# Kernel optimization log

Measured on AMD Instinct MI355X. Metric: run time of the kernel, lower is better.

Reference implementation:

```python
import jax, jax.numpy as jnp
import numpy as np

N = 100000
E = 1600000
C_IN = 128
C_OUT = 128
EPS = 1e-5


def setup_inputs() -> dict:
    key = jax.random.key(0)
    ks = jax.random.split(key, 8)
    x = jax.random.normal(ks[0], (N, C_IN), dtype=jnp.float32)
    edge_index = jax.random.randint(ks[1], (2, E), 0, N, dtype=jnp.int64)
    s_proj = 1.0 / np.sqrt(C_IN)
    s_out = 1.0 / np.sqrt(C_IN)
    W_proj = jax.random.uniform(ks[2], (C_IN, C_IN), jnp.float32, -s_proj, s_proj)
    b_proj = jax.random.uniform(ks[3], (C_IN,), jnp.float32, -s_proj, s_proj)
    W_l = jax.random.uniform(ks[4], (C_OUT, C_IN), jnp.float32, -s_out, s_out)
    b_l = jax.random.uniform(ks[5], (C_OUT,), jnp.float32, -s_out, s_out)
    W_r = jax.random.uniform(ks[6], (C_OUT, C_IN), jnp.float32, -s_out, s_out)
    gamma = jnp.ones((C_OUT,), jnp.float32)
    beta = jnp.zeros((C_OUT,), jnp.float32)
    return {"x": x, "edge_index": edge_index, "W_proj": W_proj, "b_proj": b_proj,
            "W_l": W_l, "b_l": b_l, "W_r": W_r, "gamma": gamma, "beta": beta}


def reference(x, edge_index, W_proj, b_proj, W_l, b_l, W_r, gamma, beta):
    # SAGEConv(project=True, aggr='sum'): project+ReLU source features per node,
    # gather along edges, scatter-sum at targets, then lin_l(agg) + lin_r(x_root).
    src, dst = edge_index[0], edge_index[1]
    h = jax.nn.relu(x @ W_proj.T + b_proj)            # [N, C_IN]
    msg = h[src]                                       # [E, C_IN] edge gather
    agg = jax.ops.segment_sum(msg, dst, num_segments=N)  # [N, C_IN]
    out = agg @ W_l.T + b_l + x @ W_r.T                # [N, C_OUT] (root uses unprojected x)
    # LayerNorm(c_out)
    mu = jnp.mean(out, axis=-1, keepdims=True)
    var = jnp.var(out, axis=-1, keepdims=True)
    return (out - mu) * jax.lax.rsqrt(var + EPS) * gamma + beta
```

## Files before the change

### kernel.cpp

```cpp
#include <hip/hip_runtime.h>
#include <stdint.h>

#define NN 100000
#define NE 1600000
#define C  128
#define NB 782
#define CAP 4096
#define SB_SHIFT 13
#define MB 782
#define P1B 250
#define MBO 782

typedef __attribute__((ext_vector_type(8))) short short8;
typedef __attribute__((ext_vector_type(4))) float f32x4;

__device__ __forceinline__ float bf2f(uint16_t u) {
  union { uint32_t u; float f; } v; v.u = ((uint32_t)u) << 16; return v.f;
}
__device__ __forceinline__ uint16_t f2bf(float f) {
  union { float f; uint32_t u; } v; v.f = f;
  uint32_t r = v.u + 0x7fffu + ((v.u >> 16) & 1u);
  return (uint16_t)(r >> 16);
}
__device__ __forceinline__ float2 bf2x2(uint32_t u) {
  return make_float2(bf2f((uint16_t)u), bf2f((uint16_t)(u >> 16)));
}

__global__ __launch_bounds__(256) void cast3_k(
    const float* __restrict__ a, const float* __restrict__ b, const float* __restrict__ c,
    uint16_t* __restrict__ oa, uint16_t* __restrict__ ob, uint16_t* __restrict__ oc)
{
  int i = blockIdx.x * 256 + threadIdx.x;
  int which = i >> 12, j = i & 4095;
  const float* s = which == 0 ? a : (which == 1 ? b : c);
  uint16_t* d    = which == 0 ? oa : (which == 1 ? ob : oc);
  float4 v = ((const float4*)s)[j];
  uint2 p;
  p.x = (uint32_t)f2bf(v.x) | ((uint32_t)f2bf(v.y) << 16);
  p.y = (uint32_t)f2bf(v.z) | ((uint32_t)f2bf(v.w) << 16);
  ((uint2*)d)[j] = p;
}


__global__ __launch_bounds__(512) void fused_front_k(
    const float* __restrict__ x, const uint16_t* __restrict__ wpb,
    const uint16_t* __restrict__ wrb,
    const float* __restrict__ bp, const float* __restrict__ bl,
    uint16_t* __restrict__ h, uint16_t* __restrict__ rb,
    const int* __restrict__ esrc, const int* __restrict__ edst,
    int* __restrict__ gcnt, uint32_t* __restrict__ ebuf)
{
  extern __shared__ uint8_t slds[];
  const int t = threadIdx.x;

  if (blockIdx.x < MB) {
#pragma unroll
    for (int qq = 0; qq < 8; ++qq) {
      int ci = qq * 512 + t;
      int m  = ci >> 11;
      int cj = ci & 2047;
      int cl = cj >> 4, k16 = cj & 15;
      const uint16_t* wsrc = m == 0 ? wpb : wrb;
      *(short8*)(slds + m * 32768 + cl * 256 + ((k16 ^ (cl & 15)) << 4)) =
          *(const short8*)(wsrc + cj * 8);
    }
    __syncthreads();

    const int w = t >> 6, lane = t & 63;
    const int tile_m0 = blockIdx.x * 128;
    const int r16 = lane & 15, g = lane >> 4;
    const int row = tile_m0 + w * 16 + r16;
    const int arow = row < NN ? row : NN - 1;

    short8 a[4];
    const float* xp = x + (size_t)arow * C + g * 8;
#pragma unroll
    for (int kk = 0; kk < 4; ++kk) {
      float4 u = *(const float4*)(xp + kk * 32);
      float4 v = *(const float4*)(xp + kk * 32 + 4);
      short8 av;
      av[0] = (short)f2bf(u.x); av[1] = (short)f2bf(u.y);
      av[2] = (short)f2bf(u.z); av[3] = (short)f2bf(u.w);
      av[4] = (short)f2bf(v.x); av[5] = (short)f2bf(v.y);
      av[6] = (short)f2bf(v.z); av[7] = (short)f2bf(v.w);
      a[kk] = av;
    }

    f32x4 hp[8], hr[8];
#pragma unroll
    for (int nt = 0; nt < 8; ++nt) {
      f32x4 p = {0.f, 0.f, 0.f, 0.f};
      f32x4 r = {0.f, 0.f, 0.f, 0.f};
      const int cidx = nt * 16 + r16;
      const uint8_t* rbp = slds + cidx * 256;
      const uint8_t* rbr = slds + 32768 + cidx * 256;
#pragma unroll
      for (int kk = 0; kk < 4; ++kk) {
        int slot = (((kk << 2) + g) ^ (cidx & 15)) << 4;
        p = __builtin_amdgcn_mfma_f32_16x16x32_bf16(*(const short8*)(rbp + slot), a[kk], p, 0, 0, 0);
        r = __builtin_amdgcn_mfma_f32_16x16x32_bf16(*(const short8*)(rbr + slot), a[kk], r, 0, 0, 0);
      }
      hp[nt] = p; hr[nt] = r;
    }
    __syncthreads();

    const int lrow = w * 16 + r16;
#pragma unroll
    for (int nt = 0; nt < 8; ++nt) {
      const int col0 = nt * 16 + g * 4;
      float4 bp4 = *(const float4*)(bp + col0);
      float4 bl4 = *(const float4*)(bl + col0);
      float h0 = hp[nt][0] + bp4.x, h1 = hp[nt][1] + bp4.y;
      float h2 = hp[nt][2] + bp4.z, h3 = hp[nt][3] + bp4.w;
      h0 = h0 > 0.f ? h0 : 0.f; h1 = h1 > 0.f ? h1 : 0.f;
      h2 = h2 > 0.f ? h2 : 0.f; h3 = h3 > 0.f ? h3 : 0.f;
      uint2 ph, pr;
      ph.x = (uint32_t)f2bf(h0) | ((uint32_t)f2bf(h1) << 16);
      ph.y = (uint32_t)f2bf(h2) | ((uint32_t)f2bf(h3) << 16);
      pr.x = (uint32_t)f2bf(hr[nt][0] + bl4.x) | ((uint32_t)f2bf(hr[nt][1] + bl4.y) << 16);
      pr.y = (uint32_t)f2bf(hr[nt][2] + bl4.z) | ((uint32_t)f2bf(hr[nt][3] + bl4.w) << 16);
      const int ioff = (col0 * 2) ^ ((lrow & 15) << 4);
      *(uint2*)(slds + lrow * 256 + ioff) = ph;
      *(uint2*)(slds + 32768 + lrow * 256 + ioff) = pr;
    }
    __syncthreads();

#pragma unroll
    for (int i = 0; i < 4; ++i) {
      const int ofs = i * 8192 + t * 16;
      const int trow = ofs >> 8;
      const int inrow = ofs & 255;
      const int grow = tile_m0 + trow;
      const int phys = (trow << 8) + (inrow ^ ((trow & 15) << 4));
      if (grow < NN) {
        *(uint4*)(h  + (size_t)grow * C + (inrow >> 1)) = *(const uint4*)(slds + phys);
        *(uint4*)(rb + (size_t)grow * C + (inrow >> 1)) = *(const uint4*)(slds + 32768 + phys);
      }
    }
  } else {
    int* bh = (int*)slds;
    int* gb = bh + NB;
    const int blk = blockIdx.x - MB;
    const int base = blk * 6400;

    for (int i = t; i < NB; i += 512) bh[i] = 0;

    const int4* ed4 = (const int4*)(edst + base);
    const int4* es4 = (const int4*)(esrc + base);
    int4 dv[4], sv[4];
    bool val[4];
#pragma unroll
    for (int k = 0; k < 4; ++k) {
      int i = t + k * 512;
      val[k] = (i < 1600);
      if (val[k]) { dv[k] = ed4[i]; sv[k] = es4[i]; }
    }
    __syncthreads();

#pragma unroll
    for (int k = 0; k < 4; ++k) if (val[k]) {
      atomicAdd(&bh[dv[k].x >> 7], 1); atomicAdd(&bh[dv[k].y >> 7], 1);
      atomicAdd(&bh[dv[k].z >> 7], 1); atomicAdd(&bh[dv[k].w >> 7], 1);
    }
    __syncthreads();

    for (int i = t; i < NB; i += 512) {
      int c = bh[i];
      gb[i] = c ? atomicAdd(&gcnt[i], c) : 0;
      bh[i] = 0;
    }
    __syncthreads();

#define P1_SCATTER(d, s) do { \
      int bb = (d) >> 7; \
      int o = atomicAdd(&bh[bb], 1); \
      int pos = gb[bb] + o; \
      if (pos < CAP) ebuf[(size_t)bb * CAP + pos] = ((uint32_t)((d) & 127) << 17) | (uint32_t)(s); \
    } while (0)

#pragma unroll
    for (int k = 0; k < 4; ++k) if (val[k]) {
      P1_SCATTER(dv[k].x, sv[k].x); P1_SCATTER(dv[k].y, sv[k].y);
      P1_SCATTER(dv[k].z, sv[k].z); P1_SCATTER(dv[k].w, sv[k].w);
    }
#undef P1_SCATTER
  }
}

__global__ __launch_bounds__(256) void phase2_k(
    const uint32_t* __restrict__ ebuf, const int* __restrict__ gcnt,
    int* __restrict__ ssrc, int2* __restrict__ sdeg)
{
  __shared__ uint32_t raw[CAP];
  __shared__ int lout[CAP];
  __shared__ int cnt2[128 * 16];
  __shared__ int nd[128];
  __shared__ int psum[256];
  const int b = blockIdx.x, t = threadIdx.x;
  const int n0 = b * 128;

  int acc = 0;
  for (int i = t; i < b; i += 256) acc += gcnt[i];
  psum[t] = acc;
  __syncthreads();
  for (int off = 128; off > 0; off >>= 1) {
    if (t < off) psum[t] += psum[t + off];
    __syncthreads();
  }
  const int base = psum[0];
  int cnt = gcnt[b]; if (cnt > CAP) cnt = CAP;

  for (int i = t; i < 128 * 16; i += 256) cnt2[i] = 0;
  __syncthreads();
  for (int i = t; i < cnt; i += 256) {
    uint32_t v = ebuf[(size_t)b * CAP + i];
    raw[i] = v;
    atomicAdd(&cnt2[(v >> 17) * 16 + ((v & 0x1FFFFu) >> SB_SHIFT)], 1);
  }
  __syncthreads();

  int deg_t = 0;
  if (t < 128) {
#pragma unroll
    for (int i = 0; i < 16; ++i) deg_t += cnt2[t * 16 + i];
    nd[t] = deg_t;
  }
  __syncthreads();
  for (int off = 1; off < 128; off <<= 1) {
    int v = 0;
    if (t < 128 && t >= off) v = nd[t - off];
    __syncthreads();
    if (t < 128) nd[t] += v;
    __syncthreads();
  }
  if (t < 128) {
    int pref = nd[t] - deg_t;
    if (n0 + t < NN) sdeg[n0 + t] = make_int2(base + pref, deg_t);
    int run = pref;
#pragma unroll
    for (int i = 0; i < 16; ++i) { int c = cnt2[t * 16 + i]; cnt2[t * 16 + i] = run; run += c; }
  }
  __syncthreads();
  for (int i = t; i < cnt; i += 256) {
    uint32_t v = raw[i];
    int o = atomicAdd(&cnt2[(v >> 17) * 16 + ((v & 0x1FFFFu) >> SB_SHIFT)], 1);
    lout[o] = (int)(v & 0x1FFFFu);
  }
  __syncthreads();
  for (int i = t; i < cnt; i += 256) ssrc[base + i] = lout[i];
}

__global__ __launch_bounds__(256) void aggregate_k(
    const uint16_t* __restrict__ h, const int* __restrict__ ssrc,
    const int2* __restrict__ sdeg, uint16_t* __restrict__ agg)
{
  const int wid = (blockIdx.x * 256 + threadIdx.x) >> 6;
  if (wid >= NN) return;
  const int lane = threadIdx.x & 63;
  const int q = lane >> 4;
  const int l16 = lane & 15;
  const int2 sd = sdeg[wid];
  const int s0 = sd.x, cnt = sd.y;
  const size_t choff = (size_t)l16 * 8;
  float2 a0 = {0.f, 0.f}, a1 = {0.f, 0.f}, a2 = {0.f, 0.f}, a3 = {0.f, 0.f};

#define ACC8(v) do { \
    a0 += bf2x2((v).x); a1 += bf2x2((v).y); \
    a2 += bf2x2((v).z); a3 += bf2x2((v).w); \
  } while (0)

  if (cnt > 0) {
    int e0 = ssrc[s0 + ((q      < cnt) ? q      : cnt - 1)];
    int e1 = ssrc[s0 + ((q + 4  < cnt) ? q + 4  : cnt - 1)];
    int e2 = ssrc[s0 + ((q + 8  < cnt) ? q + 8  : cnt - 1)];
    int e3 = ssrc[s0 + ((q + 12 < cnt) ? q + 12 : cnt - 1)];
    for (int j = 0; j < cnt; j += 16) {
      uint4 v0 = *(const uint4*)(h + (size_t)e0 * C + choff);
      uint4 v1 = *(const uint4*)(h + (size_t)e1 * C + choff);
      uint4 v2 = *(const uint4*)(h + (size_t)e2 * C + choff);
      uint4 v3 = *(const uint4*)(h + (size_t)e3 * C + choff);
      const int jn = j + 16;
      if (jn < cnt) {
        e0 = ssrc[s0 + ((jn + q      < cnt) ? jn + q      : cnt - 1)];
        e1 = ssrc[s0 + ((jn + q + 4  < cnt) ? jn + q + 4  : cnt - 1)];
        e2 = ssrc[s0 + ((jn + q + 8  < cnt) ? jn + q + 8  : cnt - 1)];
        e3 = ssrc[s0 + ((jn + q + 12 < cnt) ? jn + q + 12 : cnt - 1)];
      }
      if (j + q      < cnt) ACC8(v0);
      if (j + q + 4  < cnt) ACC8(v1);
      if (j + q + 8  < cnt) ACC8(v2);
      if (j + q + 12 < cnt) ACC8(v3);
    }
  }
#undef ACC8

#pragma unroll
  for (int msk = 16; msk <= 32; msk <<= 1) {
    a0.x += __shfl_xor(a0.x, msk, 64); a0.y += __shfl_xor(a0.y, msk, 64);
    a1.x += __shfl_xor(a1.x, msk, 64); a1.y += __shfl_xor(a1.y, msk, 64);
    a2.x += __shfl_xor(a2.x, msk, 64); a2.y += __shfl_xor(a2.y, msk, 64);
    a3.x += __shfl_xor(a3.x, msk, 64); a3.y += __shfl_xor(a3.y, msk, 64);
  }
  if (q == 0) {
    uint4 p;
    p.x = (uint32_t)f2bf(a0.x) | ((uint32_t)f2bf(a0.y) << 16);
    p.y = (uint32_t)f2bf(a1.x) | ((uint32_t)f2bf(a1.y) << 16);
    p.z = (uint32_t)f2bf(a2.x) | ((uint32_t)f2bf(a2.y) << 16);
    p.w = (uint32_t)f2bf(a3.x) | ((uint32_t)f2bf(a3.y) << 16);
    *(uint4*)(agg + (size_t)wid * C + choff) = p;
  }
}

__global__ __launch_bounds__(512) void gemm_out_k(
    const uint16_t* __restrict__ aggb, const uint16_t* __restrict__ rb,
    const uint16_t* __restrict__ wlb, const float* __restrict__ gamma,
    const float* __restrict__ beta, float* __restrict__ out)
{
  __shared__ uint8_t wl[32768];
  const int t = threadIdx.x;
#pragma unroll
  for (int qq = 0; qq < 4; ++qq) {
    int ci = qq * 512 + t;
    int c = ci >> 4, k16 = ci & 15;
    *(short8*)(wl + c * 256 + ((k16 ^ (c & 15)) << 4)) = *(const short8*)(wlb + ci * 8);
  }
  __syncthreads();

  const int w = t >> 6, lane = t & 63;
  const int tile_m = blockIdx.x * 128 + w * 16;
  if (tile_m >= NN) return;
  const int r16 = lane & 15, g = lane >> 4;

  const int row = tile_m + r16;
  const int arow = row < NN ? row : NN - 1;
  short8 a0[4];
  const uint16_t* p0 = aggb + (size_t)arow * C + g * 8;
#pragma unroll
  for (int kk = 0; kk < 4; ++kk) a0[kk] = *(const short8*)(p0 + kk * 32);

  f32x4 acc[8];
  float s1 = 0.f, s2 = 0.f;
#pragma unroll
  for (int nt = 0; nt < 8; ++nt) {
    f32x4 c4 = {0.f, 0.f, 0.f, 0.f};
    const int c = nt * 16 + r16;
    const uint8_t* rbl = wl + c * 256;
#pragma unroll
    for (int kk = 0; kk < 4; ++kk) {
      short8 b = *(const short8*)(rbl + ((((kk << 2) + g) ^ (c & 15)) << 4));
      c4 = __builtin_amdgcn_mfma_f32_16x16x32_bf16(b, a0[kk], c4, 0, 0, 0);
    }
    const int col0 = nt * 16 + g * 4;
    uint2 rv = *(const uint2*)(rb + (size_t)arow * C + col0);
    float2 r01 = bf2x2(rv.x), r23 = bf2x2(rv.y);
    c4[0] += r01.x; c4[1] += r01.y; c4[2] += r23.x; c4[3] += r23.y;
#pragma unroll
    for (int rr = 0; rr < 4; ++rr) { s1 += c4[rr]; s2 += c4[rr] * c4[rr]; }
    acc[nt] = c4;
  }

  s1 += __shfl_xor(s1, 16, 64); s2 += __shfl_xor(s2, 16, 64);
  s1 += __shfl_xor(s1, 32, 64); s2 += __shfl_xor(s2, 32, 64);
  const float mean = s1 * (1.f / C);
  const float var = s2 * (1.f / C) - mean * mean;
  const float rstd = rsqrtf(var + 1e-5f);

  if (row < NN) {
#pragma unroll
    for (int nt = 0; nt < 8; ++nt) {
      const int col0 = nt * 16 + g * 4;
      float4 gm = *(const float4*)(gamma + col0);
      float4 bt = *(const float4*)(beta + col0);
      float4 o;
      o.x = (acc[nt][0] - mean) * rstd * gm.x + bt.x;
      o.y = (acc[nt][1] - mean) * rstd * gm.y + bt.y;
      o.z = (acc[nt][2] - mean) * rstd * gm.z + bt.z;
      o.w = (acc[nt][3] - mean) * rstd * gm.w + bt.w;
      *(float4*)(out + (size_t)row * C + col0) = o;
    }
  }
}

extern "C" void kernel_launch(void* const* d_in, const int* in_sizes, int n_in,
                              void* d_out, int out_size, void* d_ws, size_t ws_size,
                              hipStream_t stream)
{
  const float* x        = (const float*)d_in[0];
  const int* ei         = (const int*)d_in[1];
  const float* Wp       = (const float*)d_in[2];
  const float* bp       = (const float*)d_in[3];
  const float* Wl       = (const float*)d_in[4];
  const float* bl       = (const float*)d_in[5];
  const float* Wr       = (const float*)d_in[6];
  const float* gamma    = (const float*)d_in[7];
  const float* beta     = (const float*)d_in[8];
  float* out            = (float*)d_out;

  char* ws = (char*)d_ws;
  uint16_t* rb   = (uint16_t*)(ws + 0);
  uint16_t* h    = (uint16_t*)(ws + 25600000);
  uint32_t* ebuf = (uint32_t*)(ws + 51200000);
  uint16_t* aggb = (uint16_t*)(ws + 51200000);
  uint16_t* wpb  = (uint16_t*)(ws + 76800000);
  uint16_t* wlb  = (uint16_t*)(ws + 76832768);
  uint16_t* wrb  = (uint16_t*)(ws + 76865536);
  int2* sdeg     = (int2*)(ws + 76898304);
  int* gcnt      = (int*)(ws + 77698304);
  int* ssrc      = (int*)(ws + 78102400);

  const int* esrc = ei;
  const int* edst = ei + NE;

  hipMemsetAsync(gcnt, 0, NB * sizeof(int), stream);

  cast3_k<<<48, 256, 0, stream>>>(Wp, Wl, Wr, wpb, wlb, wrb);

  fused_front_k<<<MB + P1B, 512, 65536, stream>>>(
      x, wpb, wrb, bp, bl, h, rb, esrc, edst, gcnt, ebuf);

  phase2_k<<<NB, 256, 0, stream>>>(ebuf, gcnt, ssrc, sdeg);

  aggregate_k<<<(NN + 3) / 4, 256, 0, stream>>>(h, ssrc, sdeg, aggb);

  gemm_out_k<<<MBO, 512, 0, stream>>>(aggb, rb, wlb, gamma, beta, out);
}
```

Before: 141.0 us.

## Move root GEMM x@W_r into output GEMM, drop rb buffer; split aggregate tail

The root projection x@W_r.T, previously computed in the front kernel and stored as a bf16 intermediate, is now computed in the output GEMM. That kernel rereads x in fp32, converts it to bf16 and accumulates both GEMMs into the same MFMA accumulators. This removes writing and rereading a 25.6MB intermediate, and cuts front-kernel LDS from 64KB to 32KB. The output kernel now needs 64KB of LDS and reads 51MB of fp32 x. The aggregate kernel also gets an unpredicated main loop over full 16-edge chunks plus a separate remainder step, removing per-iteration clamping and predication.

```diff
diff --git a/kernel.cpp b/kernel.cpp
--- a/kernel.cpp
+++ b/kernel.cpp
@@ -25,6 +25,16 @@
 __device__ __forceinline__ float2 bf2x2(uint32_t u) {
   return make_float2(bf2f((uint16_t)u), bf2f((uint16_t)(u >> 16)));
 }
+__device__ __forceinline__ short8 cvt_row8(const float* p) {
+  float4 u = *(const float4*)p;
+  float4 v = *(const float4*)(p + 4);
+  short8 av;
+  av[0] = (short)f2bf(u.x); av[1] = (short)f2bf(u.y);
+  av[2] = (short)f2bf(u.z); av[3] = (short)f2bf(u.w);
+  av[4] = (short)f2bf(v.x); av[5] = (short)f2bf(v.y);
+  av[6] = (short)f2bf(v.z); av[7] = (short)f2bf(v.w);
+  return av;
+}
 
 __global__ __launch_bounds__(256) void cast3_k(
     const float* __restrict__ a, const float* __restrict__ b, const float* __restrict__ c,
@@ -44,9 +54,7 @@
 
 __global__ __launch_bounds__(512) void fused_front_k(
     const float* __restrict__ x, const uint16_t* __restrict__ wpb,
-    const uint16_t* __restrict__ wrb,
-    const float* __restrict__ bp, const float* __restrict__ bl,
-    uint16_t* __restrict__ h, uint16_t* __restrict__ rb,
+    const float* __restrict__ bp, uint16_t* __restrict__ h,
     const int* __restrict__ esrc, const int* __restrict__ edst,
     int* __restrict__ gcnt, uint32_t* __restrict__ ebuf)
 {
@@ -55,14 +63,11 @@
 
   if (blockIdx.x < MB) {
 #pragma unroll
-    for (int qq = 0; qq < 8; ++qq) {
+    for (int qq = 0; qq < 4; ++qq) {
       int ci = qq * 512 + t;
-      int m  = ci >> 11;
-      int cj = ci & 2047;
-      int cl = cj >> 4, k16 = cj & 15;
-      const uint16_t* wsrc = m == 0 ? wpb : wrb;
-      *(short8*)(slds + m * 32768 + cl * 256 + ((k16 ^ (cl & 15)) << 4)) =
-          *(const short8*)(wsrc + cj * 8);
+      int cl = ci >> 4, k16 = ci & 15;
+      *(short8*)(slds + cl * 256 + ((k16 ^ (cl & 15)) << 4)) =
+          *(const short8*)(wpb + ci * 8);
     }
     __syncthreads();
 
@@ -75,32 +80,20 @@
     short8 a[4];
     const float* xp = x + (size_t)arow * C + g * 8;
 #pragma unroll
-    for (int kk = 0; kk < 4; ++kk) {
-      float4 u = *(const float4*)(xp + kk * 32);
-      float4 v = *(const float4*)(xp + kk * 32 + 4);
-      short8 av;
-      av[0] = (short)f2bf(u.x); av[1] = (short)f2bf(u.y);
-      av[2] = (short)f2bf(u.z); av[3] = (short)f2bf(u.w);
-      av[4] = (short)f2bf(v.x); av[5] = (short)f2bf(v.y);
-      av[6] = (short)f2bf(v.z); av[7] = (short)f2bf(v.w);
-      a[kk] = av;
-    }
-
-    f32x4 hp[8], hr[8];
+    for (int kk = 0; kk < 4; ++kk) a[kk] = cvt_row8(xp + kk * 32);
+
+    f32x4 hp[8];
 #pragma unroll
     for (int nt = 0; nt < 8; ++nt) {
       f32x4 p = {0.f, 0.f, 0.f, 0.f};
-      f32x4 r = {0.f, 0.f, 0.f, 0.f};
       const int cidx = nt * 16 + r16;
       const uint8_t* rbp = slds + cidx * 256;
-      const uint8_t* rbr = slds + 32768 + cidx * 256;
 #pragma unroll
       for (int kk = 0; kk < 4; ++kk) {
         int slot = (((kk << 2) + g) ^ (cidx & 15)) << 4;
         p = __builtin_amdgcn_mfma_f32_16x16x32_bf16(*(const short8*)(rbp + slot), a[kk], p, 0, 0, 0);
-        r = __builtin_amdgcn_mfma_f32_16x16x32_bf16(*(const short8*)(rbr + slot), a[kk], r, 0, 0, 0);
       }
-      hp[nt] = p; hr[nt] = r;
+      hp[nt] = p;
     }
     __syncthreads();
 
@@ -109,19 +102,14 @@
     for (int nt = 0; nt < 8; ++nt) {
       const int col0 = nt * 16 + g * 4;
       float4 bp4 = *(const float4*)(bp + col0);
-      float4 bl4 = *(const float4*)(bl + col0);
       float h0 = hp[nt][0] + bp4.x, h1 = hp[nt][1] + bp4.y;
       float h2 = hp[nt][2] + bp4.z, h3 = hp[nt][3] + bp4.w;
       h0 = h0 > 0.f ? h0 : 0.f; h1 = h1 > 0.f ? h1 : 0.f;
       h2 = h2 > 0.f ? h2 : 0.f; h3 = h3 > 0.f ? h3 : 0.f;
-      uint2 ph, pr;
+      uint2 ph;
       ph.x = (uint32_t)f2bf(h0) | ((uint32_t)f2bf(h1) << 16);
       ph.y = (uint32_t)f2bf(h2) | ((uint32_t)f2bf(h3) << 16);
-      pr.x = (uint32_t)f2bf(hr[nt][0] + bl4.x) | ((uint32_t)f2bf(hr[nt][1] + bl4.y) << 16);
-      pr.y = (uint32_t)f2bf(hr[nt][2] + bl4.z) | ((uint32_t)f2bf(hr[nt][3] + bl4.w) << 16);
-      const int ioff = (col0 * 2) ^ ((lrow & 15) << 4);
-      *(uint2*)(slds + lrow * 256 + ioff) = ph;
-      *(uint2*)(slds + 32768 + lrow * 256 + ioff) = pr;
+      *(uint2*)(slds + lrow * 256 + ((col0 * 2) ^ ((lrow & 15) << 4))) = ph;
     }
     __syncthreads();
 
@@ -131,11 +119,9 @@
       const int trow = ofs >> 8;
       const int inrow = ofs & 255;
       const int grow = tile_m0 + trow;
-      const int phys = (trow << 8) + (inrow ^ ((trow & 15) << 4));
-      if (grow < NN) {
-        *(uint4*)(h  + (size_t)grow * C + (inrow >> 1)) = *(const uint4*)(slds + phys);
-        *(uint4*)(rb + (size_t)grow * C + (inrow >> 1)) = *(const uint4*)(slds + 32768 + phys);
-      }
+      if (grow < NN)
+        *(uint4*)(h + (size_t)grow * C + (inrow >> 1)) =
+            *(const uint4*)(slds + (trow << 8) + (inrow ^ ((trow & 15) << 4)));
     }
   } else {
     int* bh = (int*)slds;
@@ -269,28 +255,45 @@
     a2 += bf2x2((v).z); a3 += bf2x2((v).w); \
   } while (0)
 
-  if (cnt > 0) {
-    int e0 = ssrc[s0 + ((q      < cnt) ? q      : cnt - 1)];
-    int e1 = ssrc[s0 + ((q + 4  < cnt) ? q + 4  : cnt - 1)];
-    int e2 = ssrc[s0 + ((q + 8  < cnt) ? q + 8  : cnt - 1)];
-    int e3 = ssrc[s0 + ((q + 12 < cnt) ? q + 12 : cnt - 1)];
-    for (int j = 0; j < cnt; j += 16) {
+  int j = 0;
+  if (cnt >= 16) {
+    int e0 = ssrc[s0 + q];
+    int e1 = ssrc[s0 + 4 + q];
+    int e2 = ssrc[s0 + 8 + q];
+    int e3 = ssrc[s0 + 12 + q];
+    for (; j + 16 <= cnt;) {
       uint4 v0 = *(const uint4*)(h + (size_t)e0 * C + choff);
       uint4 v1 = *(const uint4*)(h + (size_t)e1 * C + choff);
       uint4 v2 = *(const uint4*)(h + (size_t)e2 * C + choff);
       uint4 v3 = *(const uint4*)(h + (size_t)e3 * C + choff);
-      const int jn = j + 16;
-      if (jn < cnt) {
-        e0 = ssrc[s0 + ((jn + q      < cnt) ? jn + q      : cnt - 1)];
-        e1 = ssrc[s0 + ((jn + q + 4  < cnt) ? jn + q + 4  : cnt - 1)];
-        e2 = ssrc[s0 + ((jn + q + 8  < cnt) ? jn + q + 8  : cnt - 1)];
-        e3 = ssrc[s0 + ((jn + q + 12 < cnt) ? jn + q + 12 : cnt - 1)];
+      j += 16;
+      if (j + 16 <= cnt) {
+        e0 = ssrc[s0 + j + q];
+        e1 = ssrc[s0 + j + 4 + q];
+        e2 = ssrc[s0 + j + 8 + q];
+        e3 = ssrc[s0 + j + 12 + q];
       }
-      if (j + q      < cnt) ACC8(v0);
-      if (j + q + 4  < cnt) ACC8(v1);
-      if (j + q + 8  < cnt) ACC8(v2);
-      if (j + q + 12 < cnt) ACC8(v3);
-    }
+      ACC8(v0); ACC8(v1); ACC8(v2); ACC8(v3);
+    }
+  }
+  const int rem = cnt - j;
+  if (rem > 0) {
+    int i0 = j + ((q      < rem) ? q      : 0);
+    int i1 = j + ((q + 4  < rem) ? q + 4  : 0);
+    int i2 = j + ((q + 8  < rem) ? q + 8  : 0);
+    int i3 = j + ((q + 12 < rem) ? q + 12 : 0);
+    int e0 = ssrc[s0 + i0];
+    int e1 = ssrc[s0 + i1];
+    int e2 = ssrc[s0 + i2];
+    int e3 = ssrc[s0 + i3];
+    uint4 v0 = *(const uint4*)(h + (size_t)e0 * C + choff);
+    uint4 v1 = *(const uint4*)(h + (size_t)e1 * C + choff);
+    uint4 v2 = *(const uint4*)(h + (size_t)e2 * C + choff);
+    uint4 v3 = *(const uint4*)(h + (size_t)e3 * C + choff);
+    if (q < rem)      ACC8(v0);
+    if (q + 4 < rem)  ACC8(v1);
+    if (q + 8 < rem)  ACC8(v2);
+    if (q + 12 < rem) ACC8(v3);
   }
 #undef ACC8
 
@@ -312,17 +315,22 @@
 }
 
 __global__ __launch_bounds__(512) void gemm_out_k(
-    const uint16_t* __restrict__ aggb, const uint16_t* __restrict__ rb,
-    const uint16_t* __restrict__ wlb, const float* __restrict__ gamma,
+    const uint16_t* __restrict__ aggb, const float* __restrict__ x,
+    const uint16_t* __restrict__ wlb, const uint16_t* __restrict__ wrb,
+    const float* __restrict__ bl, const float* __restrict__ gamma,
     const float* __restrict__ beta, float* __restrict__ out)
 {
-  __shared__ uint8_t wl[32768];
+  extern __shared__ uint8_t slds[];
   const int t = threadIdx.x;
 #pragma unroll
-  for (int qq = 0; qq < 4; ++qq) {
+  for (int qq = 0; qq < 8; ++qq) {
     int ci = qq * 512 + t;
-    int c = ci >> 4, k16 = ci & 15;
-    *(short8*)(wl + c * 256 + ((k16 ^ (c & 15)) << 4)) = *(const short8*)(wlb + ci * 8);
+    int m  = ci >> 11;
+    int cj = ci & 2047;
+    int cl = cj >> 4, k16 = cj & 15;
+    const uint16_t* wsrc = m == 0 ? wlb : wrb;
+    *(short8*)(slds + m * 32768 + cl * 256 + ((k16 ^ (cl & 15)) << 4)) =
+        *(const short8*)(wsrc + cj * 8);
   }
   __syncthreads();
 
@@ -333,10 +341,14 @@
 
   const int row = tile_m + r16;
   const int arow = row < NN ? row : NN - 1;
-  short8 a0[4];
+  short8 a0[4], a1[4];
   const uint16_t* p0 = aggb + (size_t)arow * C + g * 8;
-#pragma unroll
-  for (int kk = 0; kk < 4; ++kk) a0[kk] = *(const short8*)(p0 + kk * 32);
+  const float* xp = x + (size_t)arow * C + g * 8;
+#pragma unroll
+  for (int kk = 0; kk < 4; ++kk) {
+    a0[kk] = *(const short8*)(p0 + kk * 32);
+    a1[kk] = cvt_row8(xp + kk * 32);
+  }
 
   f32x4 acc[8];
   float s1 = 0.f, s2 = 0.f;
@@ -344,16 +356,17 @@
   for (int nt = 0; nt < 8; ++nt) {
     f32x4 c4 = {0.f, 0.f, 0.f, 0.f};
     const int c = nt * 16 + r16;
-    const uint8_t* rbl = wl + c * 256;
+    const uint8_t* rbl = slds + c * 256;
+    const uint8_t* rbr = slds + 32768 + c * 256;
 #pragma unroll
     for (int kk = 0; kk < 4; ++kk) {
-      short8 b = *(const short8*)(rbl + ((((kk << 2) + g) ^ (c & 15)) << 4));
-      c4 = __builtin_amdgcn_mfma_f32_16x16x32_bf16(b, a0[kk], c4, 0, 0, 0);
+      int slot = (((kk << 2) + g) ^ (c & 15)) << 4;
+      c4 = __builtin_amdgcn_mfma_f32_16x16x32_bf16(*(const short8*)(rbl + slot), a0[kk], c4, 0, 0, 0);
+      c4 = __builtin_amdgcn_mfma_f32_16x16x32_bf16(*(const short8*)(rbr + slot), a1[kk], c4, 0, 0, 0);
     }
     const int col0 = nt * 16 + g * 4;
-    uint2 rv = *(const uint2*)(rb + (size_t)arow * C + col0);
-    float2 r01 = bf2x2(rv.x), r23 = bf2x2(rv.y);
-    c4[0] += r01.x; c4[1] += r01.y; c4[2] += r23.x; c4[3] += r23.y;
+    float4 bl4 = *(const float4*)(bl + col0);
+    c4[0] += bl4.x; c4[1] += bl4.y; c4[2] += bl4.z; c4[3] += bl4.w;
 #pragma unroll
     for (int rr = 0; rr < 4; ++rr) { s1 += c4[rr]; s2 += c4[rr] * c4[rr]; }
     acc[nt] = c4;
@@ -397,10 +410,9 @@
   float* out            = (float*)d_out;
 
   char* ws = (char*)d_ws;
-  uint16_t* rb   = (uint16_t*)(ws + 0);
-  uint16_t* h    = (uint16_t*)(ws + 25600000);
-  uint32_t* ebuf = (uint32_t*)(ws + 51200000);
-  uint16_t* aggb = (uint16_t*)(ws + 51200000);
+  uint16_t* h    = (uint16_t*)(ws + 0);
+  uint32_t* ebuf = (uint32_t*)(ws + 25600000);
+  uint16_t* aggb = (uint16_t*)(ws + 25600000);
   uint16_t* wpb  = (uint16_t*)(ws + 76800000);
   uint16_t* wlb  = (uint16_t*)(ws + 76832768);
   uint16_t* wrb  = (uint16_t*)(ws + 76865536);
@@ -415,12 +427,12 @@
 
   cast3_k<<<48, 256, 0, stream>>>(Wp, Wl, Wr, wpb, wlb, wrb);
 
-  fused_front_k<<<MB + P1B, 512, 65536, stream>>>(
-      x, wpb, wrb, bp, bl, h, rb, esrc, edst, gcnt, ebuf);
+  fused_front_k<<<MB + P1B, 512, 32768, stream>>>(
+      x, wpb, bp, h, esrc, edst, gcnt, ebuf);
 
   phase2_k<<<NB, 256, 0, stream>>>(ebuf, gcnt, ssrc, sdeg);
 
   aggregate_k<<<(NN + 3) / 4, 256, 0, stream>>>(h, ssrc, sdeg, aggb);
 
-  gemm_out_k<<<MBO, 512, 0, stream>>>(aggb, rb, wlb, gamma, beta, out);
-}
+  gemm_out_k<<<MBO, 512, 65536, stream>>>(aggb, x, wlb, wrb, bl, gamma, beta, out);
+}
```

Result: slower. 144.2 us (+2.3%).
